# Kernel optimization log

Measured on AMD Instinct MI355X. Metric: run time of the kernel, lower is better.

The kernel has to match this reference:

```python
import jax, jax.numpy as jnp
import numpy as np

N_NODES = 100000
N_EDGES = 3200000
IN_CH = 256


def setup_inputs() -> dict:
    key = jax.random.key(0)
    ks = jax.random.split(key, 8)
    x = jax.random.normal(ks[0], (N_NODES, IN_CH), dtype=jnp.float32)
    edge_index = jax.random.randint(ks[1], (2, N_EDGES), 0, N_NODES, dtype=jnp.int64)
    alpha = jnp.ones((), dtype=jnp.float32)
    beta = jnp.ones((), dtype=jnp.float32)
    s = 1.0 / np.sqrt(IN_CH)
    W_mlp = jax.random.normal(ks[2], (1, IN_CH), dtype=jnp.float32) * s
    W_lin = jax.random.normal(ks[3], (1, IN_CH), dtype=jnp.float32) * s
    W_gcn = jax.random.normal(ks[4], (1, IN_CH), dtype=jnp.float32) * s
    W_att = jax.random.normal(ks[5], (3, 3), dtype=jnp.float32) * (1.0 / np.sqrt(3))
    b_att = jax.random.normal(ks[6], (3,), dtype=jnp.float32) * 0.1
    return {"x": x, "edge_index": edge_index, "alpha": alpha, "beta": beta,
            "W_mlp": W_mlp, "W_lin": W_lin, "W_gcn": W_gcn,
            "W_att": W_att, "b_att": b_att}


def _gcn_conv(x, edge_index, W_gcn, num_nodes):
    # PyG GCNConv: add self-loops, symmetric normalization, no bias.
    loop = jnp.arange(num_nodes, dtype=edge_index.dtype)
    row = jnp.concatenate([edge_index[0], loop])  # source
    col = jnp.concatenate([edge_index[1], loop])  # target
    deg = jax.ops.segment_sum(jnp.ones_like(col, dtype=x.dtype), col,
                              num_segments=num_nodes)
    dinv = jnp.where(deg > 0, jax.lax.rsqrt(deg), 0.0)
    norm = dinv[row] * dinv[col]                  # [E+N]
    xw = x @ W_gcn.T                               # [N, 1]
    msg = norm[:, None] * xw[row]                  # [E+N, 1]
    return jax.ops.segment_sum(msg, col, num_segments=num_nodes)  # [N, 1]


def reference(x, edge_index, alpha, beta, W_mlp, W_lin, W_gcn, W_att, b_att):
    num_nodes = x.shape[0]
    # score1: in-degree based
    deg = jax.ops.segment_sum(jnp.ones((edge_index.shape[1],), dtype=x.dtype),
                              edge_index[1], num_segments=num_nodes)
    score1 = jax.nn.sigmoid(alpha * jnp.sqrt(deg) + beta)           # [N]
    # score2: tiny MLP
    score2 = jax.nn.sigmoid((x @ W_mlp.T)[:, 0])                    # [N]
    # score3: GCNConv + linear
    gcn_out = _gcn_conv(x, edge_index, W_gcn, num_nodes)            # [N,1]
    score3 = jax.nn.sigmoid((gcn_out + x @ W_lin.T)[:, 0])          # [N]
    scores = jnp.stack([score1, score2, score3], axis=1)            # [N,3]
    weight = jax.nn.softmax(scores @ W_att.T + b_att, axis=1)       # [N,3]
    fitness = jnp.sum(weight * scores, axis=1)                      # [N]
    return fitness
```

## Files before the change

### kernel.cpp

```cpp
#include <hip/hip_runtime.h>
#include <math.h>

#define N_CH    256
#define SBSHIFT 11
#define SBN     2048
#define NSMAX   64
#define CH      4096

__device__ __forceinline__ float sigmoidf_(float v) {
    return 1.0f / (1.0f + expf(-v));
}

__device__ __forceinline__ void build_tables(const int* sbT, int ns,
                                             int* sbsL, int* cstL) {
    if (threadIdx.x == 0) {
        int run = 0, c = 0;
        for (int i = 0; i < ns; ++i) {
            sbsL[i] = run;
            cstL[i] = c;
            int len = sbT[i];
            run += len;
            c += (len + CH - 1) / CH;
        }
        sbsL[ns] = run;
        cstL[ns] = c;
    }
}

__global__ __launch_bounds__(256) void dots_hist_kernel(
    const float* __restrict__ x,
    const float* __restrict__ Wmlp, const float* __restrict__ Wlin,
    const float* __restrict__ Wgcn, const int* __restrict__ dst,
    float* __restrict__ s2dot, float* __restrict__ s3lin, float* __restrict__ xw,
    int* __restrict__ H1,
    int n_nodes, int n_edges, int ns, int nch)
{
    __shared__ int h[NSMAX];
    if ((int)blockIdx.x < nch) {
        int c = blockIdx.x;
        if (threadIdx.x < NSMAX) h[threadIdx.x] = 0;
        __syncthreads();
        int start = c * CH;
        #pragma unroll
        for (int m = 0; m < 4; ++m) {
            int e = start + (m * 256 + (int)threadIdx.x) * 4;
            if (e + 3 < n_edges) {
                int4 d4 = *(const int4*)(dst + e);
                atomicAdd(&h[d4.x >> SBSHIFT], 1);
                atomicAdd(&h[d4.y >> SBSHIFT], 1);
                atomicAdd(&h[d4.z >> SBSHIFT], 1);
                atomicAdd(&h[d4.w >> SBSHIFT], 1);
            } else {
                for (int ee = e; ee < n_edges && ee >= 0; ++ee)
                    atomicAdd(&h[dst[ee] >> SBSHIFT], 1);
            }
        }
        __syncthreads();
        if (threadIdx.x < (unsigned)ns)
            H1[(size_t)threadIdx.x * nch + c] = h[threadIdx.x];
        return;
    }

    int wid  = ((int)blockIdx.x - nch) * 4 + ((int)threadIdx.x >> 6);
    int lane = threadIdx.x & 63;
    if (wid >= n_nodes) return;

    const float4* xr = (const float4*)(x + (size_t)wid * N_CH);
    float4 v  = xr[lane];
    float4 wm = ((const float4*)Wmlp)[lane];
    float4 wl = ((const float4*)Wlin)[lane];
    float4 wg = ((const float4*)Wgcn)[lane];

    float d0 = v.x*wm.x + v.y*wm.y + v.z*wm.z + v.w*wm.w;
    float d1 = v.x*wl.x + v.y*wl.y + v.z*wl.z + v.w*wl.w;
    float d2 = v.x*wg.x + v.y*wg.y + v.z*wg.z + v.w*wg.w;

    #pragma unroll
    for (int off = 32; off; off >>= 1) {
        d0 += __shfl_down(d0, off, 64);
        d1 += __shfl_down(d1, off, 64);
        d2 += __shfl_down(d2, off, 64);
    }
    if (lane == 0) { s2dot[wid] = d0; s3lin[wid] = d1; xw[wid] = d2; }
}

__global__ __launch_bounds__(1024) void scanA_kernel(
    const int* __restrict__ H1, int* __restrict__ O, int* __restrict__ sbT,
    int nch)
{
    __shared__ int s[1024];
    int sb = blockIdx.x, t = threadIdx.x;
    int v = (t < nch) ? H1[(size_t)sb * nch + t] : 0;
    s[t] = v;
    __syncthreads();
    for (int off = 1; off < 1024; off <<= 1) {
        int a = s[t];
        int b = (t >= off) ? s[t - off] : 0;
        __syncthreads();
        s[t] = a + b;
        __syncthreads();
    }
    if (t < nch) O[(size_t)sb * nch + t] = s[t] - v;
    if (t == 1023) sbT[sb] = s[1023];
}

__global__ __launch_bounds__(256) void scatter_kernel(
    const int* __restrict__ src, const int* __restrict__ dst,
    const int* __restrict__ sbT, const int* __restrict__ O,
    int* __restrict__ cpack, int n_edges, int ns, int nch)
{
    __shared__ int sbsL[NSMAX + 1], cstL[NSMAX + 1];
    __shared__ int pos0[NSMAX];
    __shared__ int lp[NSMAX + 1];
    __shared__ int h[NSMAX];
    __shared__ int sorted[CH];

    int c = blockIdx.x;
    build_tables(sbT, ns, sbsL, cstL);
    if (threadIdx.x < NSMAX) h[threadIdx.x] = 0;
    __syncthreads();
    if (threadIdx.x < (unsigned)ns)
        pos0[threadIdx.x] = sbsL[threadIdx.x] + O[(size_t)threadIdx.x * nch + c];

    int start = c * CH;
    int cnt = n_edges - start; if (cnt > CH) cnt = CH;

    int4 s4[4], d4[4];
    #pragma unroll
    for (int m = 0; m < 4; ++m) {
        int e = start + (m * 256 + (int)threadIdx.x) * 4;
        if (e + 3 < n_edges) {
            s4[m] = *(const int4*)(src + e);
            d4[m] = *(const int4*)(dst + e);
            atomicAdd(&h[d4[m].x >> SBSHIFT], 1);
            atomicAdd(&h[d4[m].y >> SBSHIFT], 1);
            atomicAdd(&h[d4[m].z >> SBSHIFT], 1);
            atomicAdd(&h[d4[m].w >> SBSHIFT], 1);
        } else {
            s4[m] = make_int4(-1, -1, -1, -1);
            int* sp = (int*)&s4[m]; int* dp = (int*)&d4[m];
            for (int j = 0; j < 4; ++j) {
                int ee = e + j;
                if (ee < n_edges && ee >= 0) {
                    sp[j] = src[ee]; dp[j] = dst[ee];
                    atomicAdd(&h[dp[j] >> SBSHIFT], 1);
                }
            }
        }
    }
    __syncthreads();
    if (threadIdx.x == 0) {
        int run = 0;
        for (int i = 0; i < ns; ++i) { lp[i] = run; run += h[i]; }
        lp[ns] = run;
    }
    __syncthreads();
    if (threadIdx.x < NSMAX) h[threadIdx.x] = 0;
    __syncthreads();
    #pragma unroll
    for (int m = 0; m < 4; ++m) {
        int* sp = (int*)&s4[m]; int* dp = (int*)&d4[m];
        #pragma unroll
        for (int j = 0; j < 4; ++j) {
            if (sp[j] >= 0) {
                int d = dp[j];
                int sb = d >> SBSHIFT;
                int r = atomicAdd(&h[sb], 1);
                sorted[lp[sb] + r] = sp[j] | ((d & (SBN - 1)) << 17);
            }
        }
    }
    __syncthreads();
    for (int p = threadIdx.x; p < cnt; p += 256) {
        int lo = 0, hi = ns;
        while (hi - lo > 1) { int mid = (lo + hi) >> 1; if (lp[mid] <= p) lo = mid; else hi = mid; }
        cpack[pos0[lo] + (p - lp[lo])] = sorted[p];
    }
}

__global__ __launch_bounds__(256) void chunkDeg_kernel(
    const int* __restrict__ cpack, const int* __restrict__ sbT,
    int* __restrict__ partialD, int ns)
{
    __shared__ int sbsL[NSMAX + 1], cstL[NSMAX + 1];
    __shared__ int cnt[SBN];
    build_tables(sbT, ns, sbsL, cstL);
    for (int i = threadIdx.x; i < SBN; i += 256) cnt[i] = 0;
    __syncthreads();
    int c = blockIdx.x;
    if (c >= cstL[ns]) return;
    int lo = 0, hi = ns;
    while (hi - lo > 1) { int mid = (lo + hi) >> 1; if (cstL[mid] <= c) lo = mid; else hi = mid; }
    int sb = lo;
    int i0 = c - cstL[sb];
    int base = sbsL[sb] + i0 * CH;
    int len = sbsL[sb + 1] - base; if (len > CH) len = CH;

    #pragma unroll
    for (int m = 0; m < 4; ++m) {
        int e = (m * 256 + (int)threadIdx.x) * 4;
        if (e + 3 < len) {
            int4 w4 = *(const int4*)(cpack + base + e);
            atomicAdd(&cnt[w4.x >> 17], 1);
            atomicAdd(&cnt[w4.y >> 17], 1);
            atomicAdd(&cnt[w4.z >> 17], 1);
            atomicAdd(&cnt[w4.w >> 17], 1);
        } else {
            for (int ee = e; ee < len && ee >= 0; ++ee)
                atomicAdd(&cnt[cpack[base + ee] >> 17], 1);
        }
    }
    __syncthreads();
    int* row = partialD + (size_t)c * SBN;
    for (int i = threadIdx.x; i < SBN; i += 256) row[i] = cnt[i];
}

__global__ __launch_bounds__(256) void reduceDeg_kernel(
    const int* __restrict__ partialD, const int* __restrict__ sbT,
    const float* __restrict__ xw,
    float* __restrict__ degf, float* __restrict__ dinv, float* __restrict__ sxw,
    int n_nodes, int ns)
{
    __shared__ int sbsL[NSMAX + 1], cstL[NSMAX + 1];
    build_tables(sbT, ns, sbsL, cstL);
    __syncthreads();
    int i = blockIdx.x * 256 + threadIdx.x;
    if (i >= n_nodes) return;
    int sb = i >> SBSHIFT, li = i & (SBN - 1);
    int c0 = cstL[sb], c1 = cstL[sb + 1];
    int d = 0;
    for (int c = c0; c < c1; ++c) d += partialD[(size_t)c * SBN + li];
    float df = (float)d;
    degf[i] = df;
    float di = rsqrtf(df + 1.0f);
    dinv[i] = di;
    sxw[i]  = di * xw[i];
}

__global__ __launch_bounds__(256) void chunkAcc_kernel(
    const int* __restrict__ cpack, const int* __restrict__ sbT,
    const float* __restrict__ sxw, float* __restrict__ partialF, int ns)
{
    __shared__ int sbsL[NSMAX + 1], cstL[NSMAX + 1];
    __shared__ float facc[SBN];
    build_tables(sbT, ns, sbsL, cstL);
    for (int i = threadIdx.x; i < SBN; i += 256) facc[i] = 0.0f;
    __syncthreads();
    int c = blockIdx.x;
    if (c >= cstL[ns]) return;
    int lo = 0, hi = ns;
    while (hi - lo > 1) { int mid = (lo + hi) >> 1; if (cstL[mid] <= c) lo = mid; else hi = mid; }
    int sb = lo;
    int i0 = c - cstL[sb];
    int base = sbsL[sb] + i0 * CH;
    int len = sbsL[sb + 1] - base; if (len > CH) len = CH;

    #pragma unroll
    for (int m = 0; m < 4; ++m) {
        int e = (m * 256 + (int)threadIdx.x) * 4;
        if (e + 3 < len) {
            int4 w4 = *(const int4*)(cpack + base + e);
            atomicAdd(&facc[w4.x >> 17], sxw[w4.x & 0x1FFFF]);
            atomicAdd(&facc[w4.y >> 17], sxw[w4.y & 0x1FFFF]);
            atomicAdd(&facc[w4.z >> 17], sxw[w4.z & 0x1FFFF]);
            atomicAdd(&facc[w4.w >> 17], sxw[w4.w & 0x1FFFF]);
        } else {
            for (int ee = e; ee < len && ee >= 0; ++ee) {
                int w = cpack[base + ee];
                atomicAdd(&facc[w >> 17], sxw[w & 0x1FFFF]);
            }
        }
    }
    __syncthreads();
    float* row = partialF + (size_t)c * SBN;
    for (int i = threadIdx.x; i < SBN; i += 256) row[i] = facc[i];
}

__global__ __launch_bounds__(256) void reduceFinal_kernel(
    const float* __restrict__ partialF, const int* __restrict__ sbT,
    const float* __restrict__ degf, const float* __restrict__ dinv,
    const float* __restrict__ xw, const float* __restrict__ s2dot,
    const float* __restrict__ s3lin,
    const float* __restrict__ alpha, const float* __restrict__ beta,
    const float* __restrict__ Watt, const float* __restrict__ batt,
    float* __restrict__ out, int n_nodes, int ns)
{
    __shared__ int sbsL[NSMAX + 1], cstL[NSMAX + 1];
    build_tables(sbT, ns, sbsL, cstL);
    __syncthreads();
    int i = blockIdx.x * 256 + threadIdx.x;
    if (i >= n_nodes) return;
    int sb = i >> SBSHIFT, li = i & (SBN - 1);
    int c0 = cstL[sb], c1 = cstL[sb + 1];
    float acc = 0.0f;
    for (int c = c0; c < c1; ++c) acc += partialF[(size_t)c * SBN + li];

    float dn = dinv[i];
    float g  = acc * dn + dn * dn * xw[i];
    float s1 = sigmoidf_(alpha[0] * sqrtf(degf[i]) + beta[0]);
    float s2 = sigmoidf_(s2dot[i]);
    float s3 = sigmoidf_(g + s3lin[i]);

    float z0 = Watt[0]*s1 + Watt[1]*s2 + Watt[2]*s3 + batt[0];
    float z1 = Watt[3]*s1 + Watt[4]*s2 + Watt[5]*s3 + batt[1];
    float z2 = Watt[6]*s1 + Watt[7]*s2 + Watt[8]*s3 + batt[2];

    float m  = fmaxf(z0, fmaxf(z1, z2));
    float e0 = expf(z0 - m), e1 = expf(z1 - m), e2 = expf(z2 - m);
    float inv = 1.0f / (e0 + e1 + e2);
    out[i] = (e0 * s1 + e1 * s2 + e2 * s3) * inv;
}

extern "C" void kernel_launch(void* const* d_in, const int* in_sizes, int n_in,
                              void* d_out, int out_size, void* d_ws, size_t ws_size,
                              hipStream_t stream) {
    const float* x     = (const float*)d_in[0];
    const int*   ei    = (const int*)d_in[1];
    const float* alpha = (const float*)d_in[2];
    const float* beta  = (const float*)d_in[3];
    const float* Wmlp  = (const float*)d_in[4];
    const float* Wlin  = (const float*)d_in[5];
    const float* Wgcn  = (const float*)d_in[6];
    const float* Watt  = (const float*)d_in[7];
    const float* batt  = (const float*)d_in[8];
    float* out = (float*)d_out;

    int n_nodes = in_sizes[0] / N_CH;
    int n_edges = in_sizes[1] / 2;
    const int* src = ei;
    const int* dst = ei + n_edges;

    int ns  = (n_nodes + SBN - 1) >> SBSHIFT;
    int nch = (n_edges + CH - 1) / CH;
    int maxChunks = nch + ns;

    size_t off = 0;
    int*   cpack    = (int*)d_ws;          off += (((size_t)n_edges + 1023) & ~(size_t)1023);
    int*   H1       = (int*)d_ws + off;    off += (((size_t)ns * nch + 1023) & ~(size_t)1023);
    int*   O        = (int*)d_ws + off;    off += (((size_t)ns * nch + 1023) & ~(size_t)1023);
    int*   sbT      = (int*)d_ws + off;    off += 128;
    int*   partialD = (int*)d_ws + off;    off += (size_t)maxChunks * SBN;
    float* partialF = (float*)d_ws + off;  off += (size_t)maxChunks * SBN;
    float* s2dot    = (float*)d_ws + off;  off += (((size_t)n_nodes + 1023) & ~(size_t)1023);
    float* s3lin    = (float*)d_ws + off;  off += (((size_t)n_nodes + 1023) & ~(size_t)1023);
    float* xw       = (float*)d_ws + off;  off += (((size_t)n_nodes + 1023) & ~(size_t)1023);
    float* degf     = (float*)d_ws + off;  off += (((size_t)n_nodes + 1023) & ~(size_t)1023);
    float* dinv     = (float*)d_ws + off;  off += (((size_t)n_nodes + 1023) & ~(size_t)1023);
    float* sxw      = (float*)d_ws + off;  off += (((size_t)n_nodes + 1023) & ~(size_t)1023);

    int dotsBlocks = (n_nodes + 3) / 4;
    dots_hist_kernel<<<nch + dotsBlocks, 256, 0, stream>>>(
        x, Wmlp, Wlin, Wgcn, dst, s2dot, s3lin, xw, H1,
        n_nodes, n_edges, ns, nch);

    scanA_kernel<<<ns, 1024, 0, stream>>>(H1, O, sbT, nch);

    scatter_kernel<<<nch, 256, 0, stream>>>(src, dst, sbT, O, cpack,
                                            n_edges, ns, nch);

    chunkDeg_kernel<<<maxChunks, 256, 0, stream>>>(cpack, sbT, partialD, ns);

    reduceDeg_kernel<<<(n_nodes + 255) / 256, 256, 0, stream>>>(
        partialD, sbT, xw, degf, dinv, sxw, n_nodes, ns);

    chunkAcc_kernel<<<maxChunks, 256, 0, stream>>>(cpack, sbT, sxw, partialF, ns);

    reduceFinal_kernel<<<(n_nodes + 255) / 256, 256, 0, stream>>>(
        partialF, sbT, degf, dinv, xw, s2dot, s3lin,
        alpha, beta, Watt, batt, out, n_nodes, ns);
}
```

Before: 244.5 us.

## Fuse reduction passes via last-block pattern and replace scan with atomic cursors

Drops the per-superbucket scan kernel. Chunk offsets now come from atomic cursor reservations in the scatter kernel, with a tiny seed kernel that builds the prefix tables once. The degree and accumulate reductions are folded into the chunk kernels using a last-block-done counter per superbucket, which cuts the pipeline from seven launches to five plus a memset. The dot-product kernel also processes 8 nodes per wave instead of one. In exchange, the ordering of edges within a superbucket is no longer deterministic, and the final per-superbucket reductions run on fewer blocks.

```diff
diff --git a/kernel.cpp b/kernel.cpp
--- a/kernel.cpp
+++ b/kernel.cpp
@@ -11,28 +11,12 @@
     return 1.0f / (1.0f + expf(-v));
 }
 
-__device__ __forceinline__ void build_tables(const int* sbT, int ns,
-                                             int* sbsL, int* cstL) {
-    if (threadIdx.x == 0) {
-        int run = 0, c = 0;
-        for (int i = 0; i < ns; ++i) {
-            sbsL[i] = run;
-            cstL[i] = c;
-            int len = sbT[i];
-            run += len;
-            c += (len + CH - 1) / CH;
-        }
-        sbsL[ns] = run;
-        cstL[ns] = c;
-    }
-}
-
 __global__ __launch_bounds__(256) void dots_hist_kernel(
     const float* __restrict__ x,
     const float* __restrict__ Wmlp, const float* __restrict__ Wlin,
     const float* __restrict__ Wgcn, const int* __restrict__ dst,
     float* __restrict__ s2dot, float* __restrict__ s3lin, float* __restrict__ xw,
-    int* __restrict__ H1,
+    int* __restrict__ H1, int* __restrict__ sbT,
     int n_nodes, int n_edges, int ns, int nch)
 {
     __shared__ int h[NSMAX];
@@ -51,122 +35,117 @@
                 atomicAdd(&h[d4.z >> SBSHIFT], 1);
                 atomicAdd(&h[d4.w >> SBSHIFT], 1);
             } else {
-                for (int ee = e; ee < n_edges && ee >= 0; ++ee)
+                int eEnd = e + 4; if (eEnd > n_edges) eEnd = n_edges;
+                for (int ee = e; ee < eEnd; ++ee)
                     atomicAdd(&h[dst[ee] >> SBSHIFT], 1);
             }
         }
         __syncthreads();
-        if (threadIdx.x < (unsigned)ns)
-            H1[(size_t)threadIdx.x * nch + c] = h[threadIdx.x];
+        if (threadIdx.x < NSMAX) {
+            int v = (threadIdx.x < (unsigned)ns) ? h[threadIdx.x] : 0;
+            H1[(size_t)c * NSMAX + threadIdx.x] = v;
+            if (v) atomicAdd(&sbT[threadIdx.x], v);
+        }
         return;
     }
 
-    int wid  = ((int)blockIdx.x - nch) * 4 + ((int)threadIdx.x >> 6);
+    int wave = ((int)blockIdx.x - nch) * 4 + ((int)threadIdx.x >> 6);
     int lane = threadIdx.x & 63;
-    if (wid >= n_nodes) return;
-
-    const float4* xr = (const float4*)(x + (size_t)wid * N_CH);
-    float4 v  = xr[lane];
+    int n0 = wave * 8;
+    if (n0 >= n_nodes) return;
     float4 wm = ((const float4*)Wmlp)[lane];
     float4 wl = ((const float4*)Wlin)[lane];
     float4 wg = ((const float4*)Wgcn)[lane];
-
-    float d0 = v.x*wm.x + v.y*wm.y + v.z*wm.z + v.w*wm.w;
-    float d1 = v.x*wl.x + v.y*wl.y + v.z*wl.z + v.w*wl.w;
-    float d2 = v.x*wg.x + v.y*wg.y + v.z*wg.z + v.w*wg.w;
-
-    #pragma unroll
-    for (int off = 32; off; off >>= 1) {
-        d0 += __shfl_down(d0, off, 64);
-        d1 += __shfl_down(d1, off, 64);
-        d2 += __shfl_down(d2, off, 64);
-    }
-    if (lane == 0) { s2dot[wid] = d0; s3lin[wid] = d1; xw[wid] = d2; }
-}
-
-__global__ __launch_bounds__(1024) void scanA_kernel(
-    const int* __restrict__ H1, int* __restrict__ O, int* __restrict__ sbT,
-    int nch)
-{
-    __shared__ int s[1024];
-    int sb = blockIdx.x, t = threadIdx.x;
-    int v = (t < nch) ? H1[(size_t)sb * nch + t] : 0;
-    s[t] = v;
-    __syncthreads();
-    for (int off = 1; off < 1024; off <<= 1) {
-        int a = s[t];
-        int b = (t >= off) ? s[t - off] : 0;
-        __syncthreads();
-        s[t] = a + b;
-        __syncthreads();
-    }
-    if (t < nch) O[(size_t)sb * nch + t] = s[t] - v;
-    if (t == 1023) sbT[sb] = s[1023];
+    int nEnd = n0 + 8; if (nEnd > n_nodes) nEnd = n_nodes;
+    for (int node = n0; node < nEnd; ++node) {
+        float4 v = ((const float4*)(x + (size_t)node * N_CH))[lane];
+        float d0 = v.x*wm.x + v.y*wm.y + v.z*wm.z + v.w*wm.w;
+        float d1 = v.x*wl.x + v.y*wl.y + v.z*wl.z + v.w*wl.w;
+        float d2 = v.x*wg.x + v.y*wg.y + v.z*wg.z + v.w*wg.w;
+        #pragma unroll
+        for (int off = 32; off; off >>= 1) {
+            d0 += __shfl_down(d0, off, 64);
+            d1 += __shfl_down(d1, off, 64);
+            d2 += __shfl_down(d2, off, 64);
+        }
+        if (lane == 0) { s2dot[node] = d0; s3lin[node] = d1; xw[node] = d2; }
+    }
+}
+
+__global__ __launch_bounds__(64) void seed_kernel(
+    const int* __restrict__ sbT, int* __restrict__ sbsG, int* __restrict__ cstG,
+    int* __restrict__ cursor, int* __restrict__ doneD, int* __restrict__ doneF,
+    int ns)
+{
+    __shared__ int sbsL[NSMAX + 1], cstL[NSMAX + 1];
+    if (threadIdx.x == 0) {
+        int run = 0, c = 0;
+        for (int i = 0; i < ns; ++i) {
+            sbsL[i] = run; cstL[i] = c;
+            int len = sbT[i];
+            run += len;
+            int nc = (len + CH - 1) / CH; if (nc < 1) nc = 1;
+            c += nc;
+        }
+        sbsL[ns] = run; cstL[ns] = c;
+    }
+    __syncthreads();
+    int t = threadIdx.x;
+    if (t <= ns) { sbsG[t] = sbsL[t]; cstG[t] = cstL[t]; }
+    if (t < ns)  { cursor[t] = sbsL[t]; doneD[t] = 0; doneF[t] = 0; }
 }
 
 __global__ __launch_bounds__(256) void scatter_kernel(
     const int* __restrict__ src, const int* __restrict__ dst,
-    const int* __restrict__ sbT, const int* __restrict__ O,
-    int* __restrict__ cpack, int n_edges, int ns, int nch)
-{
-    __shared__ int sbsL[NSMAX + 1], cstL[NSMAX + 1];
-    __shared__ int pos0[NSMAX];
+    const int* __restrict__ H1, int* __restrict__ cursor,
+    int* __restrict__ cpack, int n_edges, int ns)
+{
     __shared__ int lp[NSMAX + 1];
     __shared__ int h[NSMAX];
+    __shared__ int pos0[NSMAX];
     __shared__ int sorted[CH];
 
     int c = blockIdx.x;
-    build_tables(sbT, ns, sbsL, cstL);
-    if (threadIdx.x < NSMAX) h[threadIdx.x] = 0;
-    __syncthreads();
-    if (threadIdx.x < (unsigned)ns)
-        pos0[threadIdx.x] = sbsL[threadIdx.x] + O[(size_t)threadIdx.x * nch + c];
+    if (threadIdx.x < NSMAX) h[threadIdx.x] = H1[(size_t)c * NSMAX + threadIdx.x];
+    __syncthreads();
+    if (threadIdx.x == 0) {
+        int run = 0;
+        for (int i = 0; i < ns; ++i) { lp[i] = run; run += h[i]; }
+        lp[ns] = run;
+    }
+    __syncthreads();
+    if (threadIdx.x < (unsigned)ns) {
+        int cb = h[threadIdx.x];
+        pos0[threadIdx.x] = cb ? atomicAdd(&cursor[threadIdx.x], cb) : 0;
+        h[threadIdx.x] = 0;
+    }
+    __syncthreads();
 
     int start = c * CH;
     int cnt = n_edges - start; if (cnt > CH) cnt = CH;
 
-    int4 s4[4], d4[4];
     #pragma unroll
     for (int m = 0; m < 4; ++m) {
         int e = start + (m * 256 + (int)threadIdx.x) * 4;
         if (e + 3 < n_edges) {
-            s4[m] = *(const int4*)(src + e);
-            d4[m] = *(const int4*)(dst + e);
-            atomicAdd(&h[d4[m].x >> SBSHIFT], 1);
-            atomicAdd(&h[d4[m].y >> SBSHIFT], 1);
-            atomicAdd(&h[d4[m].z >> SBSHIFT], 1);
-            atomicAdd(&h[d4[m].w >> SBSHIFT], 1);
-        } else {
-            s4[m] = make_int4(-1, -1, -1, -1);
-            int* sp = (int*)&s4[m]; int* dp = (int*)&d4[m];
+            int4 s4 = *(const int4*)(src + e);
+            int4 d4 = *(const int4*)(dst + e);
+            int ss[4] = {s4.x, s4.y, s4.z, s4.w};
+            int dd[4] = {d4.x, d4.y, d4.z, d4.w};
+            #pragma unroll
             for (int j = 0; j < 4; ++j) {
-                int ee = e + j;
-                if (ee < n_edges && ee >= 0) {
-                    sp[j] = src[ee]; dp[j] = dst[ee];
-                    atomicAdd(&h[dp[j] >> SBSHIFT], 1);
-                }
-            }
-        }
-    }
-    __syncthreads();
-    if (threadIdx.x == 0) {
-        int run = 0;
-        for (int i = 0; i < ns; ++i) { lp[i] = run; run += h[i]; }
-        lp[ns] = run;
-    }
-    __syncthreads();
-    if (threadIdx.x < NSMAX) h[threadIdx.x] = 0;
-    __syncthreads();
-    #pragma unroll
-    for (int m = 0; m < 4; ++m) {
-        int* sp = (int*)&s4[m]; int* dp = (int*)&d4[m];
-        #pragma unroll
-        for (int j = 0; j < 4; ++j) {
-            if (sp[j] >= 0) {
-                int d = dp[j];
+                int d = dd[j];
                 int sb = d >> SBSHIFT;
                 int r = atomicAdd(&h[sb], 1);
-                sorted[lp[sb] + r] = sp[j] | ((d & (SBN - 1)) << 17);
+                sorted[lp[sb] + r] = ss[j] | ((d & (SBN - 1)) << 17);
+            }
+        } else {
+            int eEnd = e + 4; if (eEnd > n_edges) eEnd = n_edges;
+            for (int ee = e; ee < eEnd; ++ee) {
+                int d = dst[ee];
+                int sb = d >> SBSHIFT;
+                int r = atomicAdd(&h[sb], 1);
+                sorted[lp[sb] + r] = src[ee] | ((d & (SBN - 1)) << 17);
             }
         }
     }
@@ -178,27 +157,32 @@
     }
 }
 
-__global__ __launch_bounds__(256) void chunkDeg_kernel(
-    const int* __restrict__ cpack, const int* __restrict__ sbT,
-    int* __restrict__ partialD, int ns)
+__global__ __launch_bounds__(256) void chunkDegReduce_kernel(
+    const int* __restrict__ cpack, const int* __restrict__ sbsG,
+    const int* __restrict__ cstG, int* __restrict__ partialD,
+    int* __restrict__ doneD, const float* __restrict__ xw,
+    float* __restrict__ degf, float* __restrict__ dinv, float* __restrict__ sxw,
+    int n_nodes, int ns)
 {
     __shared__ int sbsL[NSMAX + 1], cstL[NSMAX + 1];
     __shared__ int cnt[SBN];
-    build_tables(sbT, ns, sbsL, cstL);
-    for (int i = threadIdx.x; i < SBN; i += 256) cnt[i] = 0;
+    __shared__ int lastFlag;
+    int t = threadIdx.x;
+    if (t <= ns) { sbsL[t] = sbsG[t]; cstL[t] = cstG[t]; }
     __syncthreads();
     int c = blockIdx.x;
     if (c >= cstL[ns]) return;
     int lo = 0, hi = ns;
     while (hi - lo > 1) { int mid = (lo + hi) >> 1; if (cstL[mid] <= c) lo = mid; else hi = mid; }
-    int sb = lo;
-    int i0 = c - cstL[sb];
+    int sb = lo, i0 = c - cstL[sb];
     int base = sbsL[sb] + i0 * CH;
-    int len = sbsL[sb + 1] - base; if (len > CH) len = CH;
-
+    int len = sbsL[sb + 1] - base; if (len > CH) len = CH; if (len < 0) len = 0;
+
+    for (int i = t; i < SBN; i += 256) cnt[i] = 0;
+    __syncthreads();
     #pragma unroll
     for (int m = 0; m < 4; ++m) {
-        int e = (m * 256 + (int)threadIdx.x) * 4;
+        int e = (m * 256 + t) * 4;
         if (e + 3 < len) {
             int4 w4 = *(const int4*)(cpack + base + e);
             atomicAdd(&cnt[w4.x >> 17], 1);
@@ -206,58 +190,65 @@
             atomicAdd(&cnt[w4.z >> 17], 1);
             atomicAdd(&cnt[w4.w >> 17], 1);
         } else {
-            for (int ee = e; ee < len && ee >= 0; ++ee)
+            int eEnd = e + 4; if (eEnd > len) eEnd = len;
+            for (int ee = e; ee < eEnd; ++ee)
                 atomicAdd(&cnt[cpack[base + ee] >> 17], 1);
         }
     }
     __syncthreads();
     int* row = partialD + (size_t)c * SBN;
-    for (int i = threadIdx.x; i < SBN; i += 256) row[i] = cnt[i];
-}
-
-__global__ __launch_bounds__(256) void reduceDeg_kernel(
-    const int* __restrict__ partialD, const int* __restrict__ sbT,
-    const float* __restrict__ xw,
-    float* __restrict__ degf, float* __restrict__ dinv, float* __restrict__ sxw,
-    int n_nodes, int ns)
-{
-    __shared__ int sbsL[NSMAX + 1], cstL[NSMAX + 1];
-    build_tables(sbT, ns, sbsL, cstL);
-    __syncthreads();
-    int i = blockIdx.x * 256 + threadIdx.x;
-    if (i >= n_nodes) return;
-    int sb = i >> SBSHIFT, li = i & (SBN - 1);
+    for (int i = t; i < SBN; i += 256) row[i] = cnt[i];
+    __threadfence();
+    if (t == 0)
+        lastFlag = (atomicAdd(&doneD[sb], 1) == (cstL[sb + 1] - cstL[sb]) - 1);
+    __syncthreads();
+    if (!lastFlag) return;
+    __threadfence();
     int c0 = cstL[sb], c1 = cstL[sb + 1];
-    int d = 0;
-    for (int c = c0; c < c1; ++c) d += partialD[(size_t)c * SBN + li];
-    float df = (float)d;
-    degf[i] = df;
-    float di = rsqrtf(df + 1.0f);
-    dinv[i] = di;
-    sxw[i]  = di * xw[i];
-}
-
-__global__ __launch_bounds__(256) void chunkAcc_kernel(
-    const int* __restrict__ cpack, const int* __restrict__ sbT,
-    const float* __restrict__ sxw, float* __restrict__ partialF, int ns)
+    int node0 = sb << SBSHIFT;
+    for (int li = t; li < SBN; li += 256) {
+        int node = node0 + li;
+        if (node >= n_nodes) break;
+        int d = 0;
+        for (int cc = c0; cc < c1; ++cc) d += partialD[(size_t)cc * SBN + li];
+        float df = (float)d;
+        degf[node] = df;
+        float di = rsqrtf(df + 1.0f);
+        dinv[node] = di;
+        sxw[node]  = di * xw[node];
+    }
+}
+
+__global__ __launch_bounds__(256) void chunkAccFinal_kernel(
+    const int* __restrict__ cpack, const int* __restrict__ sbsG,
+    const int* __restrict__ cstG, float* __restrict__ partialF,
+    int* __restrict__ doneF, const float* __restrict__ sxw,
+    const float* __restrict__ degf, const float* __restrict__ dinv,
+    const float* __restrict__ xw, const float* __restrict__ s2dot,
+    const float* __restrict__ s3lin,
+    const float* __restrict__ alpha, const float* __restrict__ beta,
+    const float* __restrict__ Watt, const float* __restrict__ batt,
+    float* __restrict__ out, int n_nodes, int ns)
 {
     __shared__ int sbsL[NSMAX + 1], cstL[NSMAX + 1];
     __shared__ float facc[SBN];
-    build_tables(sbT, ns, sbsL, cstL);
-    for (int i = threadIdx.x; i < SBN; i += 256) facc[i] = 0.0f;
+    __shared__ int lastFlag;
+    int t = threadIdx.x;
+    if (t <= ns) { sbsL[t] = sbsG[t]; cstL[t] = cstG[t]; }
     __syncthreads();
     int c = blockIdx.x;
     if (c >= cstL[ns]) return;
     int lo = 0, hi = ns;
     while (hi - lo > 1) { int mid = (lo + hi) >> 1; if (cstL[mid] <= c) lo = mid; else hi = mid; }
-    int sb = lo;
-    int i0 = c - cstL[sb];
+    int sb = lo, i0 = c - cstL[sb];
     int base = sbsL[sb] + i0 * CH;
-    int len = sbsL[sb + 1] - base; if (len > CH) len = CH;
-
+    int len = sbsL[sb + 1] - base; if (len > CH) len = CH; if (len < 0) len = 0;
+
+    for (int i = t; i < SBN; i += 256) facc[i] = 0.0f;
+    __syncthreads();
     #pragma unroll
     for (int m = 0; m < 4; ++m) {
-        int e = (m * 256 + (int)threadIdx.x) * 4;
+        int e = (m * 256 + t) * 4;
         if (e + 3 < len) {
             int4 w4 = *(const int4*)(cpack + base + e);
             atomicAdd(&facc[w4.x >> 17], sxw[w4.x & 0x1FFFF]);
@@ -265,7 +256,8 @@
             atomicAdd(&facc[w4.z >> 17], sxw[w4.z & 0x1FFFF]);
             atomicAdd(&facc[w4.w >> 17], sxw[w4.w & 0x1FFFF]);
         } else {
-            for (int ee = e; ee < len && ee >= 0; ++ee) {
+            int eEnd = e + 4; if (eEnd > len) eEnd = len;
+            for (int ee = e; ee < eEnd; ++ee) {
                 int w = cpack[base + ee];
                 atomicAdd(&facc[w >> 17], sxw[w & 0x1FFFF]);
             }
@@ -273,42 +265,37 @@
     }
     __syncthreads();
     float* row = partialF + (size_t)c * SBN;
-    for (int i = threadIdx.x; i < SBN; i += 256) row[i] = facc[i];
-}
-
-__global__ __launch_bounds__(256) void reduceFinal_kernel(
-    const float* __restrict__ partialF, const int* __restrict__ sbT,
-    const float* __restrict__ degf, const float* __restrict__ dinv,
-    const float* __restrict__ xw, const float* __restrict__ s2dot,
-    const float* __restrict__ s3lin,
-    const float* __restrict__ alpha, const float* __restrict__ beta,
-    const float* __restrict__ Watt, const float* __restrict__ batt,
-    float* __restrict__ out, int n_nodes, int ns)
-{
-    __shared__ int sbsL[NSMAX + 1], cstL[NSMAX + 1];
-    build_tables(sbT, ns, sbsL, cstL);
-    __syncthreads();
-    int i = blockIdx.x * 256 + threadIdx.x;
-    if (i >= n_nodes) return;
-    int sb = i >> SBSHIFT, li = i & (SBN - 1);
+    for (int i = t; i < SBN; i += 256) row[i] = facc[i];
+    __threadfence();
+    if (t == 0)
+        lastFlag = (atomicAdd(&doneF[sb], 1) == (cstL[sb + 1] - cstL[sb]) - 1);
+    __syncthreads();
+    if (!lastFlag) return;
+    __threadfence();
     int c0 = cstL[sb], c1 = cstL[sb + 1];
-    float acc = 0.0f;
-    for (int c = c0; c < c1; ++c) acc += partialF[(size_t)c * SBN + li];
-
-    float dn = dinv[i];
-    float g  = acc * dn + dn * dn * xw[i];
-    float s1 = sigmoidf_(alpha[0] * sqrtf(degf[i]) + beta[0]);
-    float s2 = sigmoidf_(s2dot[i]);
-    float s3 = sigmoidf_(g + s3lin[i]);
-
-    float z0 = Watt[0]*s1 + Watt[1]*s2 + Watt[2]*s3 + batt[0];
-    float z1 = Watt[3]*s1 + Watt[4]*s2 + Watt[5]*s3 + batt[1];
-    float z2 = Watt[6]*s1 + Watt[7]*s2 + Watt[8]*s3 + batt[2];
-
-    float m  = fmaxf(z0, fmaxf(z1, z2));
-    float e0 = expf(z0 - m), e1 = expf(z1 - m), e2 = expf(z2 - m);
-    float inv = 1.0f / (e0 + e1 + e2);
-    out[i] = (e0 * s1 + e1 * s2 + e2 * s3) * inv;
+    int node0 = sb << SBSHIFT;
+    float a = alpha[0], b = beta[0];
+    for (int li = t; li < SBN; li += 256) {
+        int node = node0 + li;
+        if (node >= n_nodes) break;
+        float acc = 0.0f;
+        for (int cc = c0; cc < c1; ++cc) acc += partialF[(size_t)cc * SBN + li];
+
+        float dn = dinv[node];
+        float g  = acc * dn + dn * dn * xw[node];
+        float s1 = sigmoidf_(a * sqrtf(degf[node]) + b);
+        float s2 = sigmoidf_(s2dot[node]);
+        float s3 = sigmoidf_(g + s3lin[node]);
+
+        float z0 = Watt[0]*s1 + Watt[1]*s2 + Watt[2]*s3 + batt[0];
+        float z1 = Watt[3]*s1 + Watt[4]*s2 + Watt[5]*s3 + batt[1];
+        float z2 = Watt[6]*s1 + Watt[7]*s2 + Watt[8]*s3 + batt[2];
+
+        float m  = fmaxf(z0, fmaxf(z1, z2));
+        float e0 = expf(z0 - m), e1 = expf(z1 - m), e2 = expf(z2 - m);
+        float inv = 1.0f / (e0 + e1 + e2);
+        out[node] = (e0 * s1 + e1 * s2 + e2 * s3) * inv;
+    }
 }
 
 extern "C" void kernel_launch(void* const* d_in, const int* in_sizes, int n_in,
@@ -336,9 +323,13 @@
 
     size_t off = 0;
     int*   cpack    = (int*)d_ws;          off += (((size_t)n_edges + 1023) & ~(size_t)1023);
-    int*   H1       = (int*)d_ws + off;    off += (((size_t)ns * nch + 1023) & ~(size_t)1023);
-    int*   O        = (int*)d_ws + off;    off += (((size_t)ns * nch + 1023) & ~(size_t)1023);
+    int*   H1       = (int*)d_ws + off;    off += (((size_t)nch * NSMAX + 1023) & ~(size_t)1023);
     int*   sbT      = (int*)d_ws + off;    off += 128;
+    int*   sbsG     = (int*)d_ws + off;    off += 128;
+    int*   cstG     = (int*)d_ws + off;    off += 128;
+    int*   cursor   = (int*)d_ws + off;    off += 128;
+    int*   doneD    = (int*)d_ws + off;    off += 128;
+    int*   doneF    = (int*)d_ws + off;    off += 128;
     int*   partialD = (int*)d_ws + off;    off += (size_t)maxChunks * SBN;
     float* partialF = (float*)d_ws + off;  off += (size_t)maxChunks * SBN;
     float* s2dot    = (float*)d_ws + off;  off += (((size_t)n_nodes + 1023) & ~(size_t)1023);
@@ -348,24 +339,22 @@
     float* dinv     = (float*)d_ws + off;  off += (((size_t)n_nodes + 1023) & ~(size_t)1023);
     float* sxw      = (float*)d_ws + off;  off += (((size_t)n_nodes + 1023) & ~(size_t)1023);
 
-    int dotsBlocks = (n_nodes + 3) / 4;
+    hipMemsetAsync(sbT, 0, 128 * sizeof(int), stream);
+
+    int dotsBlocks = (n_nodes + 31) / 32;
     dots_hist_kernel<<<nch + dotsBlocks, 256, 0, stream>>>(
-        x, Wmlp, Wlin, Wgcn, dst, s2dot, s3lin, xw, H1,
+        x, Wmlp, Wlin, Wgcn, dst, s2dot, s3lin, xw, H1, sbT,
         n_nodes, n_edges, ns, nch);
 
-    scanA_kernel<<<ns, 1024, 0, stream>>>(H1, O, sbT, nch);
-
-    scatter_kernel<<<nch, 256, 0, stream>>>(src, dst, sbT, O, cpack,
-                                            n_edges, ns, nch);
-
-    chunkDeg_kernel<<<maxChunks, 256, 0, stream>>>(cpack, sbT, partialD, ns);
-
-    reduceDeg_kernel<<<(n_nodes + 255) / 256, 256, 0, stream>>>(
-        partialD, sbT, xw, degf, dinv, sxw, n_nodes, ns);
-
-    chunkAcc_kernel<<<maxChunks, 256, 0, stream>>>(cpack, sbT, sxw, partialF, ns);
-
-    reduceFinal_kernel<<<(n_nodes + 255) / 256, 256, 0, stream>>>(
-        partialF, sbT, degf, dinv, xw, s2dot, s3lin,
+    seed_kernel<<<1, 64, 0, stream>>>(sbT, sbsG, cstG, cursor, doneD, doneF, ns);
+
+    scatter_kernel<<<nch, 256, 0, stream>>>(src, dst, H1, cursor, cpack,
+                                            n_edges, ns);
+
+    chunkDegReduce_kernel<<<maxChunks, 256, 0, stream>>>(
+        cpack, sbsG, cstG, partialD, doneD, xw, degf, dinv, sxw, n_nodes, ns);
+
+    chunkAccFinal_kernel<<<maxChunks, 256, 0, stream>>>(
+        cpack, sbsG, cstG, partialF, doneF, sxw, degf, dinv, xw, s2dot, s3lin,
         alpha, beta, Watt, batt, out, n_nodes, ns);
 }
```

After: 485.3 us. 1.98x slower.
